# Optimization experiments

Hardware: AMD Instinct MI355X
Metric: run time of the kernel (lower is better)

Reference implementation:

```python
import jax, jax.numpy as jnp
import numpy as np

N, E = 50000, 800000
H, V, ED = 128, 32, 64
EH = 2 * H + 2 * V          # edge MLP hidden = 320
EO = 2 * H + 2 * V          # edge MLP out (H+H+V+V) = 320
NH = 2 * H + V              # node MLP hidden = 288
NO = H + V                  # node MLP out = 160


def _ln(x, g, b, eps=1e-5):
    m = x.mean(-1, keepdims=True)
    v = ((x - m) ** 2).mean(-1, keepdims=True)
    return (x - m) * jax.lax.rsqrt(v + eps) * g + b


def setup_inputs() -> dict:
    key = jax.random.key(0)
    ks = jax.random.split(key, 12)
    s = 0.05
    return {
        "scalar_state": jax.random.normal(ks[0], (N, H), jnp.float32),
        "vector_state": jax.random.normal(ks[1], (N, 3, V), jnp.float32),
        "edge_attr": jax.random.normal(ks[2], (E, ED), jnp.float32),
        "edge_vector": jax.random.normal(ks[3], (E, 3), jnp.float32),
        "sn_g": jnp.ones((H,), jnp.float32), "sn_b": jnp.zeros((H,), jnp.float32),
        "pn_g": jnp.ones((H,), jnp.float32), "pn_b": jnp.zeros((H,), jnp.float32),
        "e_w1": jax.random.normal(ks[4], (2 * H + ED, EH), jnp.float32) * s,
        "e_b1": jnp.zeros((EH,), jnp.float32),
        "e_w2": jax.random.normal(ks[5], (EH, EO), jnp.float32) * s,
        "e_b2": jnp.zeros((EO,), jnp.float32),
        "n_w1": jax.random.normal(ks[6], (H + V, NH), jnp.float32) * s,
        "n_b1": jnp.zeros((NH,), jnp.float32),
        "n_w2": jax.random.normal(ks[7], (NH, NO), jnp.float32) * s,
        "n_b2": jnp.zeros((NO,), jnp.float32),
        "edge_index": jax.random.randint(ks[8], (2, E), 0, N, jnp.int64),
    }


def reference(scalar_state, vector_state, edge_attr, edge_vector,
              sn_g, sn_b, pn_g, pn_b,
              e_w1, e_b1, e_w2, e_b2,
              n_w1, n_b1, n_w2, n_b2, edge_index):
    tgt = edge_index[0]
    src = edge_index[1]

    # LayerNorm is per-row, so normalize once then gather (same math as gather-then-norm)
    s_norm = _ln(scalar_state, sn_g, sn_b)
    edge_in = jnp.concatenate([s_norm[tgt], s_norm[src], edge_attr], axis=-1)  # [E, 2H+ED]
    h = jax.nn.silu(edge_in @ e_w1 + e_b1)
    upd = h @ e_w2 + e_b2                                                      # [E, 2H+2V]
    sm = upd[:, :H]
    sg = upd[:, H:2 * H]
    vg = upd[:, 2 * H:2 * H + V]
    ds = upd[:, 2 * H + V:]

    sm = sm * jax.nn.sigmoid(sg)                                               # scalar message [E,H]

    # F.normalize(edge_vector, dim=-1, eps=1e-8)
    ev_norm = jnp.sqrt((edge_vector ** 2).sum(-1, keepdims=True))
    unit = edge_vector / jnp.maximum(ev_norm, 1e-8)                            # [E,3]

    src_vec = vector_state[src] * jax.nn.sigmoid(vg)[:, None, :]               # [E,3,V]
    dir_vec = unit[:, :, None] * ds[:, None, :]                                # [E,3,V]
    vmsg = src_vec + dir_vec

    # mean aggregation (index_add / counts)
    counts = jax.ops.segment_sum(jnp.ones((E,), sm.dtype), tgt, num_segments=N)
    counts = jnp.maximum(counts, 1.0)
    s_upd = jax.ops.segment_sum(sm, tgt, num_segments=N) / counts[:, None]
    v_upd = jax.ops.segment_sum(vmsg.reshape(E, 3 * V), tgt, num_segments=N).reshape(N, 3, V) / counts[:, None, None]

    scalar_state = scalar_state + s_upd
    vector_state = vector_state + v_upd

    vnorm = jnp.sqrt(jnp.maximum((vector_state ** 2).sum(axis=1), 1e-8))       # [N,V]
    node_in = jnp.concatenate([_ln(scalar_state, pn_g, pn_b), vnorm], axis=-1)
    h2 = jax.nn.silu(node_in @ n_w1 + n_b1)
    nu = h2 @ n_w2 + n_b2                                                      # [N,H+V]
    scalar_delta = nu[:, :H]
    vector_scale = nu[:, H:]

    scalar_state = scalar_state + scalar_delta
    vector_state = vector_state * (1.0 + 0.1 * jnp.tanh(vector_scale))[:, None, :]
    return scalar_state, vector_state
```

## Files before the change

kernel.cpp:

```cpp
#include <hip/hip_runtime.h>

#define N_NODES 50000
#define N_EDGES 800000

typedef __attribute__((ext_vector_type(8))) short short8;
typedef __attribute__((ext_vector_type(4))) float floatx4;
typedef __attribute__((ext_vector_type(4))) unsigned int u32x4;
typedef __attribute__((ext_vector_type(2))) __bf16 bf16x2;
typedef unsigned short ushort_t;
typedef unsigned int uint_t;

__device__ __forceinline__ uint_t pkbf(float lo, float hi){
  bf16x2 v = { (__bf16)lo, (__bf16)hi };
  return __builtin_bit_cast(uint_t, v);
}
__device__ __forceinline__ ushort_t f2bf(float f){
  return __builtin_bit_cast(ushort_t, (__bf16)f);
}
__device__ __forceinline__ float bf2f(ushort_t h){
  unsigned u = ((unsigned)h) << 16;
  return __builtin_bit_cast(float, u);
}
__device__ __forceinline__ float sigm(float x){
  return __builtin_amdgcn_rcpf(1.f + __expf(-x));
}
__device__ __forceinline__ float tanh_f(float x){
  float ax = fabsf(x);
  float t = 1.f - 2.f*__builtin_amdgcn_rcpf(__expf(2.f*ax) + 1.f);
  return copysignf(t, x);
}
__device__ __forceinline__ float waveRed(float v){
  #pragma unroll
  for (int o=32;o>0;o>>=1) v += __shfl_xor(v,o);
  return v;
}
__device__ __forceinline__ int ldIdx(const int* __restrict__ idx, long long pos, int mode){
  return mode ? idx[pos*2] : idx[pos];
}
__device__ __forceinline__ short8 as_s8(u32x4 v){ return __builtin_bit_cast(short8, v); }

__device__ __forceinline__ void gl_lds16(const ushort_t* g, ushort_t* l){
  __builtin_amdgcn_global_load_lds(
    (const __attribute__((address_space(1))) unsigned int*)(unsigned long long)(uintptr_t)g,
    (__attribute__((address_space(3))) unsigned int*)(unsigned int)(uintptr_t)l,
    16, 0, 0);
}

__device__ __forceinline__ u32x4 bfadd8(u32x4 a, u32x4 b){
  u32x4 r;
  #pragma unroll
  for (int i=0;i<4;++i){
    float alo = __builtin_bit_cast(float, a[i]<<16);
    float ahi = __builtin_bit_cast(float, a[i]&0xffff0000u);
    float blo = __builtin_bit_cast(float, b[i]<<16);
    float bhi = __builtin_bit_cast(float, b[i]&0xffff0000u);
    r[i] = pkbf(alo+blo, ahi+bhi);
  }
  return r;
}
__device__ __forceinline__ short8 pack8(floatx4 x, floatx4 y){
  u32x4 u;
  u[0] = pkbf(x[0], x[1]); u[1] = pkbf(x[2], x[3]);
  u[2] = pkbf(y[0], y[1]); u[3] = pkbf(y[2], y[3]);
  return __builtin_bit_cast(short8, u);
}


__global__ void kDetect(const int* __restrict__ idx, int* __restrict__ flag){
  if (threadIdx.x==0 && blockIdx.x==0){
    int any = 0;
    for (int i=1;i<64;i+=2) any |= idx[i];
    *flag = (any==0) ? 1 : 0;
  }
}

__global__ void kLN(const float* __restrict__ s, const float* __restrict__ g,
                    const float* __restrict__ b, ushort_t* __restrict__ out, int N){
  int wid = threadIdx.x >> 6, lane = threadIdx.x & 63;
  int n = blockIdx.x*4 + wid;
  if (n >= N) return;
  float x0 = s[(size_t)n*128 + lane], x1 = s[(size_t)n*128 + 64 + lane];
  float sum = waveRed(x0 + x1);
  float sq  = waveRed(x0*x0 + x1*x1);
  float mean = sum * (1.f/128.f);
  float var  = sq * (1.f/128.f) - mean*mean;
  float rstd = rsqrtf(var + 1e-5f);
  out[(size_t)n*128 + lane]      = f2bf((x0-mean)*rstd*g[lane] + b[lane]);
  out[(size_t)n*128 + 64 + lane] = f2bf((x1-mean)*rstd*g[64+lane] + b[64+lane]);
}

__global__ void kReorder(const float* __restrict__ W, ushort_t* __restrict__ Wp,
                         int K, int OUT){
  int total = K*OUT;
  for (int o = blockIdx.x*blockDim.x + threadIdx.x; o < total; o += gridDim.x*blockDim.x){
    int j = o & 7; int rest = o >> 3;
    int nn = rest % OUT; int qk = rest / OUT;
    int q = qk & 3, kt = qk >> 2;
    int k = kt*32 + q*8 + j;
    Wp[o] = f2bf(W[(size_t)k*OUT + nn]);
  }
}

__global__ void kReorderAB(const float* __restrict__ W, ushort_t* __restrict__ Wp){
  int total = 128*640;
  for (int o = blockIdx.x*blockDim.x + threadIdx.x; o < total; o += gridDim.x*blockDim.x){
    int j = o & 7; int rest = o >> 3;
    int nn = rest % 640; int qk = rest / 640;
    int q = qk & 3, kt = qk >> 2;
    int k = kt*32 + q*8 + j;
    float v = (nn < 320) ? W[(size_t)k*320 + nn] : W[(size_t)(128+k)*320 + (nn-320)];
    Wp[o] = f2bf(v);
  }
}


__global__ void kHist(const int* __restrict__ idx, const int* __restrict__ flagp,
                      int* __restrict__ counts){
  int mode = *flagp;
  long long e = (long long)blockIdx.x*256 + threadIdx.x;
  if (e < N_EDGES) atomicAdd(&counts[ldIdx(idx, e, mode)], 1);
}

__global__ void kScanLocal(const int* __restrict__ counts, int* __restrict__ offsets,
                           int* __restrict__ bsum, int n){
  int tid = threadIdx.x, lane = tid & 63, wid = tid >> 6;
  int i = blockIdx.x*1024 + tid;
  int x = (i<n) ? counts[i] : 0;
  int v = x;
  #pragma unroll
  for (int o=1;o<64;o<<=1){ int t = __shfl_up(v,o); if (lane>=o) v += t; }
  __shared__ int ws[16];
  if (lane==63) ws[wid] = v;
  __syncthreads();
  if (wid==0){
    int s = (lane<16) ? ws[lane] : 0;
    #pragma unroll
    for (int o=1;o<16;o<<=1){ int t = __shfl_up(s,o); if (lane>=o) s += t; }
    if (lane<16) ws[lane] = s;
  }
  __syncthreads();
  int base = wid ? ws[wid-1] : 0;
  if (i<n) offsets[i] = base + v - x;
  if (tid==1023) bsum[blockIdx.x] = ws[15];
}
__global__ void kScanSums(const int* __restrict__ bsum, int* __restrict__ bbase, int nb){
  int lane = threadIdx.x;
  int x = (lane<nb) ? bsum[lane] : 0;
  int v = x;
  #pragma unroll
  for (int o=1;o<64;o<<=1){ int t = __shfl_up(v,o); if (lane>=o) v += t; }
  if (lane<nb) bbase[lane] = v - x;
}
__global__ void kScanAdd(int* __restrict__ offsets, int* __restrict__ cursor,
                         const int* __restrict__ bbase, int n){
  int i = blockIdx.x*1024 + threadIdx.x;
  if (i<n){ int v = offsets[i] + bbase[blockIdx.x]; offsets[i]=v; cursor[i]=v; }
}

__global__ void kScatter(const int* __restrict__ idx, const int* __restrict__ flagp,
                         int* __restrict__ cursor, const float* __restrict__ edge_vector,
                         int* __restrict__ sortedE, ushort_t* __restrict__ sortedT,
                         floatx4* __restrict__ aux){
  int mode = *flagp;
  long long e = (long long)blockIdx.x*256 + threadIdx.x;
  if (e < N_EDGES){
    int t = ldIdx(idx, e, mode);
    int s = ldIdx(idx, (long long)N_EDGES + e, mode);
    float ex = edge_vector[e*3], ey = edge_vector[e*3+1], ez = edge_vector[e*3+2];
    float inr = 1.f / fmaxf(sqrtf(ex*ex+ey*ey+ez*ez), 1e-8f);
    int pos = atomicAdd(&cursor[t], 1);
    sortedE[pos] = (int)e;
    sortedT[pos] = (ushort_t)t;
    floatx4 a; a[0] = __int_as_float(s); a[1] = ex*inr; a[2] = ey*inr; a[3] = ez*inr;
    aux[pos] = a;
  }
}

__global__ __launch_bounds__(256,2) void kNodeP(
  const ushort_t* __restrict__ s_norm, const ushort_t* __restrict__ Wabp,
  const float* __restrict__ b1, ushort_t* __restrict__ P)
{
  __shared__ u32x4 sA[1024];
  __shared__ u32x4 sB[2560];
  const int tid = threadIdx.x;
  const int lane = tid & 63, wid = tid >> 6;
  const int col = lane & 15, quad = lane >> 4;
  const int nb0 = blockIdx.x * 64;

  for (int i=0;i<4;++i){
    int d = i*256 + tid;
    int m=d&15, q=(d>>4)&3, mt=(d>>6)&3, kt=d>>8;
    int node = nb0 + mt*16 + m;
    u32x4 v = {0,0,0,0};
    if (node < N_NODES) v = *(const u32x4*)(s_norm + (size_t)node*128 + (kt*4+q)*8);
    sA[d] = v;
  }

  const floatx4 zz = {0.f,0.f,0.f,0.f};
  floatx4 acc[10][4];
  #pragma unroll
  for (int i=0;i<10;++i)
    #pragma unroll
    for (int j=0;j<4;++j) acc[i][j] = zz;

  for (int kt=0; kt<4; ++kt){
    for (int i=0;i<10;++i){
      int cb = i*256 + wid*64;
      gl_lds16(Wabp + ((size_t)kt*2560 + cb + lane)*8, (ushort_t*)&sB[cb]);
    }
    __syncthreads();
    short8 a[4];
    #pragma unroll
    for (int mt=0; mt<4; ++mt)
      a[mt] = as_s8(sA[((kt*4+mt)*4+quad)*16 + col]);
    #pragma unroll
    for (int nt=0; nt<10; ++nt){
      int n = wid*160 + nt*16 + col;
      short8 b = as_s8(sB[quad*640 + n]);
      #pragma unroll
      for (int mt=0; mt<4; ++mt)
        acc[nt][mt] = __builtin_amdgcn_mfma_f32_16x16x32_bf16(a[mt], b, acc[nt][mt], 0,0,0);
    }
    __syncthreads();
  }

  #pragma unroll
  for (int nt=0; nt<10; ++nt){
    int n = wid*160 + nt*16 + col;
    float bias = (n < 320) ? b1[n] : 0.f;
    #pragma unroll
    for (int mt=0; mt<4; ++mt)
      #pragma unroll
      for (int reg=0; reg<4; ++reg){
        int node = nb0 + mt*16 + quad*4 + reg;
        if (node < N_NODES)
          P[(size_t)node*640 + n] = f2bf(acc[nt][mt][reg] + bias);
      }
  }
}

__global__ __launch_bounds__(256,4) void kEdgeMLP(
    const ushort_t* __restrict__ P, const float* __restrict__ edge_attr,
    const ushort_t* __restrict__ W1cp, const ushort_t* __restrict__ W2p,
    const float* __restrict__ b2, const int* __restrict__ sortedE,
    const ushort_t* __restrict__ sortedT, const floatx4* __restrict__ aux,
    ushort_t* __restrict__ msg)
{
  __shared__ u32x4 sA[2560];
  const int tid = threadIdx.x;
  const int lane = tid & 63, wid = tid >> 6;
  const int col = lane & 15, quad = lane >> 4;
  const long long p0 = (long long)blockIdx.x * 64;

  int ncol[5];
  ncol[0] = wid*32 + col;
  ncol[1] = ncol[0] + 16;
  ncol[2] = ncol[0] + 128;
  ncol[3] = ncol[0] + 144;
  ncol[4] = 256 + wid*16 + col;

  int eId[4];
  #pragma unroll
  for (int mt=0;mt<4;++mt) eId[mt] = sortedE[p0 + mt*16 + col];

  short8 aQ[2][4];
  #pragma unroll
  for (int kq=0; kq<2; ++kq)
    #pragma unroll
    for (int mt=0; mt<4; ++mt){
      const float* fp = edge_attr + (size_t)eId[mt]*64 + kq*32 + quad*8;
      aQ[kq][mt] = pack8(*(const floatx4*)fp, *(const floatx4*)(fp+4));
    }

  {
    const int r = wid*16 + col;
    int tgt = (int)sortedT[p0 + r];
    int src = __float_as_int(((const float*)aux)[(size_t)(p0 + r)*4]);
    const u32x4* pT = (const u32x4*)(P + (size_t)tgt*640) + quad;
    const u32x4* pS = (const u32x4*)(P + (size_t)src*640 + 320) + quad;
    #pragma unroll
    for (int i=0;i<10;++i)
      sA[i*256 + tid] = bfadd8(pT[i*4], pS[i*4]);
  }
  __syncthreads();

  const floatx4 zz = {0.f,0.f,0.f,0.f};
  floatx4 acc[5][4];
  #pragma unroll
  for (int i=0;i<5;++i)
    #pragma unroll
    for (int j=0;j<4;++j) acc[i][j] = zz;

  #pragma unroll
  for (int kq=0; kq<2; ++kq)
    #pragma unroll
    for (int nt=0; nt<5; ++nt){
      short8 b = as_s8(*(const u32x4*)(W1cp + ((size_t)(kq*4+quad)*320 + ncol[nt])*8));
      #pragma unroll
      for (int mt=0; mt<4; ++mt)
        acc[nt][mt] = __builtin_amdgcn_mfma_f32_16x16x32_bf16(aQ[kq][mt], b, acc[nt][mt], 0,0,0);
    }

  ushort_t* sH16 = (ushort_t*)sA;
  #pragma unroll
  for (int nt=0; nt<5; ++nt){
    int n = ncol[nt];
    ushort_t* hp = sH16 + (((n>>5)*256 + ((n>>3)&3)*16 + quad*4)*8 + (n&7));
    #pragma unroll
    for (int mt=0; mt<4; ++mt)
      #pragma unroll
      for (int reg=0; reg<4; ++reg){
        int a2 = mt*512 + reg*8;
        float x = acc[nt][mt][reg] + bf2f(hp[a2]);
        hp[a2] = f2bf(x * sigm(x));
      }
  }
  #pragma unroll
  for (int i=0;i<5;++i)
    #pragma unroll
    for (int j=0;j<4;++j) acc[i][j] = zz;
  __syncthreads();

  float b2c[5];
  #pragma unroll
  for (int nt=0;nt<5;++nt) b2c[nt] = b2[ncol[nt]];

  const ushort_t* w2q = W2p + (size_t)quad*320*8;
  for (int kt=0; kt<10; ++kt){
    short8 bfr[5];
    #pragma unroll
    for (int nt=0; nt<5; ++nt)
      bfr[nt] = as_s8(*(const u32x4*)(w2q + (size_t)kt*10240 + (size_t)ncol[nt]*8));
    short8 a[4];
    #pragma unroll
    for (int mt=0; mt<4; ++mt)
      a[mt] = as_s8(sA[((kt*4+mt)*4+quad)*16 + col]);
    #pragma unroll
    for (int nt=0; nt<5; ++nt)
      #pragma unroll
      for (int mt=0; mt<4; ++mt)
        acc[nt][mt] = __builtin_amdgcn_mfma_f32_16x16x32_bf16(a[mt], bfr[nt], acc[nt][mt], 0,0,0);
  }

  #pragma unroll
  for (int mt=0; mt<4; ++mt)
    #pragma unroll
    for (int reg=0; reg<4; ++reg){
      int row = mt*16 + quad*4 + reg;
      ushort_t* mrow = msg + (size_t)(p0 + row)*192;
      float a0 = acc[0][mt][reg] + b2c[0];
      float g0 = acc[2][mt][reg] + b2c[2];
      mrow[ncol[0]] = f2bf(a0 * sigm(g0));
      float a1 = acc[1][mt][reg] + b2c[1];
      float g1 = acc[3][mt][reg] + b2c[3];
      mrow[ncol[1]] = f2bf(a1 * sigm(g1));
      float v4 = acc[4][mt][reg] + b2c[4];
      float ov = (wid < 2) ? sigm(v4) : v4;
      mrow[ncol[4] - 128] = f2bf(ov);
    }
}

__global__ __launch_bounds__(128) void kAgg(
  const ushort_t* __restrict__ msg, const floatx4* __restrict__ aux,
  const int* __restrict__ counts, const int* __restrict__ offsets,
  const float* __restrict__ scalar_state, const float* __restrict__ vector_state,
  const float* __restrict__ pn_g, const float* __restrict__ pn_b,
  float* __restrict__ outS, float* __restrict__ outV, ushort_t* __restrict__ node_in)
{
  int n = blockIdx.x, t = threadIdx.x;
  int cnt = counts[n], start = offsets[n];
  int c = t >> 5, vv = t & 31;
  const ushort_t* mb = msg + (size_t)start*192;
  const floatx4* ab = aux + start;
  float accS0 = 0.f, accS1 = 0.f;
  float accV0 = 0.f, accV1 = 0.f;
  int i = 0;
  for (; i+2 <= cnt; i += 2){
    const ushort_t* r0 = mb + (size_t)i*192;
    const ushort_t* r1 = r0 + 192;
    accS0 += bf2f(__builtin_nontemporal_load(r0 + t));
    accS1 += bf2f(__builtin_nontemporal_load(r1 + t));
    if (t < 96){
      floatx4 a0 = ab[i], a1 = ab[i+1];
      int s0 = __float_as_int(a0[0]), s1 = __float_as_int(a1[0]);
      float sg0 = bf2f(__builtin_nontemporal_load(r0 + 128 + vv));
      float sg1 = bf2f(__builtin_nontemporal_load(r1 + 128 + vv));
      float d0  = bf2f(__builtin_nontemporal_load(r0 + 160 + vv));
      float d1  = bf2f(__builtin_nontemporal_load(r1 + 160 + vv));
      float sv0 = vector_state[(size_t)s0*96 + t];
      float sv1 = vector_state[(size_t)s1*96 + t];
      float uc0 = (c==0) ? a0[1] : (c==1) ? a0[2] : a0[3];
      float uc1 = (c==0) ? a1[1] : (c==1) ? a1[2] : a1[3];
      accV0 += sv0*sg0 + uc0*d0;
      accV1 += sv1*sg1 + uc1*d1;
    }
  }
  if (i < cnt){
    const ushort_t* r0 = mb + (size_t)i*192;
    accS0 += bf2f(__builtin_nontemporal_load(r0 + t));
    if (t < 96){
      floatx4 a0 = ab[i];
      int s0 = __float_as_int(a0[0]);
      float sg0 = bf2f(__builtin_nontemporal_load(r0 + 128 + vv));
      float d0  = bf2f(__builtin_nontemporal_load(r0 + 160 + vv));
      float sv0 = vector_state[(size_t)s0*96 + t];
      float uc0 = (c==0) ? a0[1] : (c==1) ? a0[2] : a0[3];
      accV0 += sv0*sg0 + uc0*d0;
    }
  }
  float accS = accS0 + accS1;
  float accV = accV0 + accV1;
  float inv = 1.f / fmaxf((float)cnt, 1.f);
  __shared__ float lv[96];
  __shared__ float pS[2], pQ[2];
  float s1 = scalar_state[(size_t)n*128 + t] + accS*inv;
  outS[(size_t)n*128 + t] = s1;
  if (t < 96){
    float v1 = vector_state[(size_t)n*96 + t] + accV*inv;
    outV[(size_t)n*96 + t] = v1;
    lv[t] = v1;
  }
  float wsum = waveRed(s1), wsq = waveRed(s1*s1);
  if ((t&63)==0){ pS[t>>6]=wsum; pQ[t>>6]=wsq; }
  __syncthreads();
  float mean = (pS[0]+pS[1]) * (1.f/128.f);
  float var  = (pQ[0]+pQ[1]) * (1.f/128.f) - mean*mean;
  float rstd = rsqrtf(var + 1e-5f);
  node_in[(size_t)n*160 + t] = f2bf((s1-mean)*rstd*pn_g[t] + pn_b[t]);
  if (t < 32){
    float a = lv[t], b = lv[32+t], d = lv[64+t];
    float vn = sqrtf(fmaxf(a*a+b*b+d*d, 1e-8f));
    node_in[(size_t)n*160 + 128 + t] = f2bf(vn);
  }
}

__global__ __launch_bounds__(256,2) void kNodeMLP(
  const ushort_t* __restrict__ node_in, const ushort_t* __restrict__ W1np,
  const ushort_t* __restrict__ W2np, const float* __restrict__ b1,
  const float* __restrict__ b2, float* __restrict__ outS, float* __restrict__ outV)
{
  __shared__ u32x4 sA[640];
  __shared__ u32x4 sH[1152];
  const int tid = threadIdx.x;
  const int lane = tid & 63, wid = tid >> 6;
  const int col = lane & 15, quad = lane >> 4;
  const int wm = wid & 1, wn = wid >> 1;
  const int rbase = blockIdx.x * 32;

  for (int d = tid; d < 640; d += 256){
    int m = d & 15, q = (d>>4)&3, mtile = (d>>6)&1, kt = d>>7;
    int r = rbase + mtile*16 + m, cc = kt*4 + q;
    u32x4 v = {0,0,0,0};
    if (r < N_NODES) v = *(const u32x4*)(node_in + (size_t)r*160 + cc*8);
    sA[d] = v;
  }
  __syncthreads();

  const floatx4 zz = {0.f,0.f,0.f,0.f};
  floatx4 acc[9];
  #pragma unroll
  for (int i=0;i<9;++i) acc[i] = zz;

  for (int kt=0; kt<5; ++kt){
    short8 a = as_s8(sA[((kt*2+wm)*4+quad)*16 + col]);
    #pragma unroll
    for (int jt=0; jt<9; ++jt){
      int n = wn*144 + jt*16 + col;
      short8 b = as_s8(*(const u32x4*)(W1np + (size_t)kt*9216 + ((size_t)quad*288 + n)*8));
      acc[jt] = __builtin_amdgcn_mfma_f32_16x16x32_bf16(a, b, acc[jt], 0,0,0);
    }
  }
  ushort_t* sH16 = (ushort_t*)sH;
  #pragma unroll
  for (int jt=0; jt<9; ++jt){
    int n = wn*144 + jt*16 + col;
    float bias = b1[n];
    int kt_h = n>>5, q_h = (n>>3)&3, j_h = n&7;
    #pragma unroll
    for (int reg=0; reg<4; ++reg){
      int ml = quad*4 + reg;
      float x = acc[jt][reg] + bias;
      float s = x * sigm(x);
      int chunk = ((kt_h*2 + wm)*4 + q_h)*16 + ml;
      sH16[chunk*8 + j_h] = f2bf(s);
    }
  }
  __syncthreads();

  floatx4 acc2[5];
  #pragma unroll
  for (int i=0;i<5;++i) acc2[i] = zz;

  for (int kt=0; kt<9; ++kt){
    short8 a = as_s8(sH[((kt*2+wm)*4+quad)*16 + col]);
    #pragma unroll
    for (int jt=0; jt<5; ++jt){
      int n = wn*80 + jt*16 + col;
      short8 b = as_s8(*(const u32x4*)(W2np + (size_t)kt*5120 + ((size_t)quad*160 + n)*8));
      acc2[jt] = __builtin_amdgcn_mfma_f32_16x16x32_bf16(a, b, acc2[jt], 0,0,0);
    }
  }

  #pragma unroll
  for (int jt=0; jt<5; ++jt){
    int n = wn*80 + jt*16 + col;
    float bias = b2[n];
    #pragma unroll
    for (int reg=0; reg<4; ++reg){
      int ml = quad*4 + reg;
      int r = rbase + wm*16 + ml;
      if (r < N_NODES){
        float val = acc2[jt][reg] + bias;
        if (n < 128){
          float* o = outS + (size_t)r*128 + n;
          *o = *o + val;
        } else {
          int vv = n - 128;
          float f = 1.f + 0.1f * tanh_f(val);
          float* o = outV + (size_t)r*96 + vv;
          o[0] *= f; o[32] *= f; o[64] *= f;
        }
      }
    }
  }
}


extern "C" void kernel_launch(void* const* d_in, const int* in_sizes, int n_in,
                              void* d_out, int out_size, void* d_ws, size_t ws_size,
                              hipStream_t stream)
{
  const float* scalar_state = (const float*)d_in[0];
  const float* vector_state = (const float*)d_in[1];
  const float* edge_attr    = (const float*)d_in[2];
  const float* edge_vector  = (const float*)d_in[3];
  const float* sn_g = (const float*)d_in[4];
  const float* sn_b = (const float*)d_in[5];
  const float* pn_g = (const float*)d_in[6];
  const float* pn_b = (const float*)d_in[7];
  const float* e_w1 = (const float*)d_in[8];
  const float* e_b1 = (const float*)d_in[9];
  const float* e_w2 = (const float*)d_in[10];
  const float* e_b2 = (const float*)d_in[11];
  const float* n_w1 = (const float*)d_in[12];
  const float* n_b1 = (const float*)d_in[13];
  const float* n_w2 = (const float*)d_in[14];
  const float* n_b2 = (const float*)d_in[15];
  const int*   eidx = (const int*)d_in[16];

  char* p = (char*)d_ws;
  auto take = [&](size_t bytes)->char*{
    char* r = p; p += (bytes + 255) & ~(size_t)255; return r;
  };
  int*      flag    = (int*)take(4);
  ushort_t* s_norm  = (ushort_t*)take((size_t)N_NODES*128*2);
  ushort_t* Wabp    = (ushort_t*)take((size_t)128*640*2);
  ushort_t* W1cp    = (ushort_t*)take((size_t)64*320*2);
  ushort_t* W2p     = (ushort_t*)take((size_t)320*320*2);
  ushort_t* W1np    = (ushort_t*)take((size_t)160*288*2);
  ushort_t* W2np    = (ushort_t*)take((size_t)288*160*2);
  int*      counts  = (int*)take((size_t)N_NODES*4);
  int*      offsets = (int*)take((size_t)N_NODES*4);
  int*      cursor  = (int*)take((size_t)N_NODES*4);
  int*      bsum    = (int*)take(64*4);
  int*      bbase   = (int*)take(64*4);
  int*      sortedE = (int*)take((size_t)N_EDGES*4);
  ushort_t* sortedT = (ushort_t*)take((size_t)N_EDGES*2);
  floatx4*  aux     = (floatx4*)take((size_t)N_EDGES*16);
  ushort_t* Pbuf    = (ushort_t*)take((size_t)N_NODES*640*2);
  ushort_t* msg     = (ushort_t*)take((size_t)N_EDGES*192*2);
  ushort_t* node_in = Pbuf;
  (void)ws_size; (void)in_sizes; (void)n_in; (void)out_size;

  float* outS = (float*)d_out;
  float* outV = outS + (size_t)N_NODES*128;

  kDetect<<<1, 64, 0, stream>>>(eidx, flag);
  kLN<<<(N_NODES+3)/4, 256, 0, stream>>>(scalar_state, sn_g, sn_b, s_norm, N_NODES);
  kReorderAB<<<160, 256, 0, stream>>>(e_w1, Wabp);
  kReorder<<<160, 256, 0, stream>>>(e_w1 + (size_t)256*320, W1cp, 64, 320);
  kReorder<<<160, 256, 0, stream>>>(e_w2, W2p, 320, 320);
  kReorder<<<160, 256, 0, stream>>>(n_w1, W1np, 160, 288);
  kReorder<<<160, 256, 0, stream>>>(n_w2, W2np, 288, 160);
  hipMemsetAsync(counts, 0, (size_t)N_NODES*4, stream);
  kHist<<<N_EDGES/256, 256, 0, stream>>>(eidx, flag, counts);
  int nsb = (N_NODES + 1023)/1024;
  kScanLocal<<<nsb, 1024, 0, stream>>>(counts, offsets, bsum, N_NODES);
  kScanSums<<<1, 64, 0, stream>>>(bsum, bbase, nsb);
  kScanAdd<<<nsb, 1024, 0, stream>>>(offsets, cursor, bbase, N_NODES);
  kScatter<<<N_EDGES/256, 256, 0, stream>>>(eidx, flag, cursor, edge_vector,
                                            sortedE, sortedT, aux);
  kNodeP<<<(N_NODES+63)/64, 256, 0, stream>>>(s_norm, Wabp, e_b1, Pbuf);
  kEdgeMLP<<<N_EDGES/64, 256, 0, stream>>>(Pbuf, edge_attr, W1cp, W2p,
                                           e_b2, sortedE, sortedT, aux, msg);
  kAgg<<<N_NODES, 128, 0, stream>>>(msg, aux, counts, offsets,
                                    scalar_state, vector_state,
                                    pn_g, pn_b, outS, outV, node_in);
  kNodeMLP<<<(N_NODES+31)/32, 256, 0, stream>>>(node_in, W1np, W2np, n_b1, n_b2, outS, outV);
}
```

Baseline: 1.140 ms.

## Fuse gathered node projections into the first-layer epilogue with transposed MFMA

Drops the separate pass that gathered the target and source node projections, added them, and staged the sums in LDS before a barrier. The MFMA operands are swapped so each lane holds four consecutive output columns, which lets the epilogue load the tgt/src projection slices directly as 8-byte vectors, add them to the accumulator, apply SiLU, and write packed bf16 into the LDS layout the second GEMM reads. This removes one LDS round trip, one barrier, and the bf16 rounding of the intermediate sum. Occupancy hint lowered from 4 to 3 blocks per CU, which gives more registers per thread but may reduce latency hiding for the scattered gathers.

```diff
diff --git a/kernel.cpp b/kernel.cpp
--- a/kernel.cpp
+++ b/kernel.cpp
@@ -6,6 +6,7 @@
 typedef __attribute__((ext_vector_type(8))) short short8;
 typedef __attribute__((ext_vector_type(4))) float floatx4;
 typedef __attribute__((ext_vector_type(4))) unsigned int u32x4;
+typedef __attribute__((ext_vector_type(2))) unsigned int u32x2;
 typedef __attribute__((ext_vector_type(2))) __bf16 bf16x2;
 typedef unsigned short ushort_t;
 typedef unsigned int uint_t;
@@ -46,18 +47,6 @@
     16, 0, 0);
 }
 
-__device__ __forceinline__ u32x4 bfadd8(u32x4 a, u32x4 b){
-  u32x4 r;
-  #pragma unroll
-  for (int i=0;i<4;++i){
-    float alo = __builtin_bit_cast(float, a[i]<<16);
-    float ahi = __builtin_bit_cast(float, a[i]&0xffff0000u);
-    float blo = __builtin_bit_cast(float, b[i]<<16);
-    float bhi = __builtin_bit_cast(float, b[i]&0xffff0000u);
-    r[i] = pkbf(alo+blo, ahi+bhi);
-  }
-  return r;
-}
 __device__ __forceinline__ short8 pack8(floatx4 x, floatx4 y){
   u32x4 u;
   u[0] = pkbf(x[0], x[1]); u[1] = pkbf(x[2], x[3]);
@@ -239,7 +228,7 @@
   }
 }
 
-__global__ __launch_bounds__(256,4) void kEdgeMLP(
+__global__ __launch_bounds__(256,3) void kEdgeMLP(
     const ushort_t* __restrict__ P, const float* __restrict__ edge_attr,
     const ushort_t* __restrict__ W1cp, const ushort_t* __restrict__ W2p,
     const float* __restrict__ b2, const int* __restrict__ sortedE,
@@ -252,12 +241,15 @@
   const int col = lane & 15, quad = lane >> 4;
   const long long p0 = (long long)blockIdx.x * 64;
 
+  int nbase[5];
+  nbase[0] = wid*32;
+  nbase[1] = nbase[0] + 16;
+  nbase[2] = nbase[0] + 128;
+  nbase[3] = nbase[0] + 144;
+  nbase[4] = 256 + wid*16;
   int ncol[5];
-  ncol[0] = wid*32 + col;
-  ncol[1] = ncol[0] + 16;
-  ncol[2] = ncol[0] + 128;
-  ncol[3] = ncol[0] + 144;
-  ncol[4] = 256 + wid*16 + col;
+  #pragma unroll
+  for (int nt=0;nt<5;++nt) ncol[nt] = nbase[nt] + col;
 
   int eId[4];
   #pragma unroll
@@ -271,18 +263,6 @@
       const float* fp = edge_attr + (size_t)eId[mt]*64 + kq*32 + quad*8;
       aQ[kq][mt] = pack8(*(const floatx4*)fp, *(const floatx4*)(fp+4));
     }
-
-  {
-    const int r = wid*16 + col;
-    int tgt = (int)sortedT[p0 + r];
-    int src = __float_as_int(((const float*)aux)[(size_t)(p0 + r)*4]);
-    const u32x4* pT = (const u32x4*)(P + (size_t)tgt*640) + quad;
-    const u32x4* pS = (const u32x4*)(P + (size_t)src*640 + 320) + quad;
-    #pragma unroll
-    for (int i=0;i<10;++i)
-      sA[i*256 + tid] = bfadd8(pT[i*4], pS[i*4]);
-  }
-  __syncthreads();
 
   const floatx4 zz = {0.f,0.f,0.f,0.f};
   floatx4 acc[5][4];
@@ -298,22 +278,32 @@
       short8 b = as_s8(*(const u32x4*)(W1cp + ((size_t)(kq*4+quad)*320 + ncol[nt])*8));
       #pragma unroll
       for (int mt=0; mt<4; ++mt)
-        acc[nt][mt] = __builtin_amdgcn_mfma_f32_16x16x32_bf16(aQ[kq][mt], b, acc[nt][mt], 0,0,0);
+        acc[nt][mt] = __builtin_amdgcn_mfma_f32_16x16x32_bf16(b, aQ[kq][mt], acc[nt][mt], 0,0,0);
     }
 
   ushort_t* sH16 = (ushort_t*)sA;
   #pragma unroll
-  for (int nt=0; nt<5; ++nt){
-    int n = ncol[nt];
-    ushort_t* hp = sH16 + (((n>>5)*256 + ((n>>3)&3)*16 + quad*4)*8 + (n&7));
-    #pragma unroll
-    for (int mt=0; mt<4; ++mt)
-      #pragma unroll
-      for (int reg=0; reg<4; ++reg){
-        int a2 = mt*512 + reg*8;
-        float x = acc[nt][mt][reg] + bf2f(hp[a2]);
-        hp[a2] = f2bf(x * sigm(x));
-      }
+  for (int mt=0; mt<4; ++mt){
+    int rr = mt*16 + col;
+    int tgt = (int)sortedT[p0 + rr];
+    int src = __float_as_int(((const float*)aux)[(size_t)(p0 + rr)*4]);
+    const ushort_t* pT = P + (size_t)tgt*640 + quad*4;
+    const ushort_t* pS = P + (size_t)src*640 + 320 + quad*4;
+    #pragma unroll
+    for (int nt=0; nt<5; ++nt){
+      int nb = nbase[nt];
+      u32x2 tp = *(const u32x2*)(pT + nb);
+      u32x2 sp = *(const u32x2*)(pS + nb);
+      float x0 = acc[nt][mt][0] + bf2f((ushort_t)(tp[0]&0xffffu)) + bf2f((ushort_t)(sp[0]&0xffffu));
+      float x1 = acc[nt][mt][1] + bf2f((ushort_t)(tp[0]>>16))     + bf2f((ushort_t)(sp[0]>>16));
+      float x2 = acc[nt][mt][2] + bf2f((ushort_t)(tp[1]&0xffffu)) + bf2f((ushort_t)(sp[1]&0xffffu));
+      float x3 = acc[nt][mt][3] + bf2f((ushort_t)(tp[1]>>16))     + bf2f((ushort_t)(sp[1]>>16));
+      u32x2 dd;
+      dd[0] = pkbf(x0 * sigm(x0), x1 * sigm(x1));
+      dd[1] = pkbf(x2 * sigm(x2), x3 * sigm(x3));
+      int c = (((nb>>5)*4 + mt)*4 + ((nb>>3)&3) + (quad>>1));
+      *(u32x2*)(sH16 + (size_t)(c*16 + col)*8 + (quad&1)*4) = dd;
+    }
   }
   #pragma unroll
   for (int i=0;i<5;++i)
```

New measurement: 1.204 ms. 5.6% more time.
